# Kernel tuning notes

Hardware: AMD Instinct MI355X
Metric: run time of the kernel (lower is better)

The kernel has to match this reference:

```python
import jax, jax.numpy as jnp
import numpy as np

B, IN_CAPS, IN_DIM = 256, 1152, 8
NUM_CAPS, DIM_VEC = 10, 16
NUM_ROUTING = 3


def squash(v, axis=-1):
    # scale = |v|^2 / (1+|v|^2) / |v|
    s2 = jnp.sum(jnp.square(v), axis=axis, keepdims=True)
    scale = s2 / (1.0 + s2) / jnp.sqrt(s2)
    return scale * v


def setup_inputs() -> dict:
    key = jax.random.key(0)
    k1, k2 = jax.random.split(key)
    inputs = jax.random.normal(k1, (B, IN_CAPS, IN_DIM), dtype=jnp.float32)
    W = jax.random.normal(k2, (IN_CAPS, NUM_CAPS, IN_DIM, DIM_VEC), dtype=jnp.float32) * 0.05
    bias = jnp.zeros((1, IN_CAPS, NUM_CAPS), dtype=jnp.float32)
    return {"inputs": inputs, "W": W, "bias": bias}


def reference(inputs, W, bias):
    # inputs_hat[b,i,j,d] = sum_e inputs[b,i,e] * W[i,j,e,d]
    hat = jnp.einsum('bie,ijed->bijd', inputs, W)  # [B, ic, nc, dv]
    b_logits = bias  # [1, ic, nc], broadcasts to [B, ic, nc] after first update
    outputs = None
    for r in range(NUM_ROUTING):
        c = jax.nn.softmax(b_logits, axis=2)            # coupling over output caps
        s = jnp.sum(c[..., None] * hat, axis=1)         # [B, nc, dv]
        outputs = squash(s)                             # [B, nc, dv]
        if r != NUM_ROUTING - 1:
            # agreement: <hat[b,i,j,:], v[b,j,:]>
            b_logits = b_logits + jnp.einsum('bijd,bjd->bij', hat, outputs)
    return outputs  # [B, num_capsule, dim_vector]
```

## Files before the change

### kernel.cpp

```cpp
#include <hip/hip_runtime.h>
#include <hip/hip_fp16.h>


#define IC 1152
#define IE 8
#define NC 10
#define DV 16
#define NB 256
#define NW (IC * NC * IE * DV)
#define SOUT (NC * DV)
#define GPB (IC / 32)
#define NBB 8
#define TPB (NBB * 64)
#define WSLOT (NC * 8 * 64)

typedef _Float16 h2 __attribute__((ext_vector_type(2)));
union WChunk { int4 v; h2 p[4]; _Float16 h[8]; };
union XFrag { int4 v; h2 p[4]; };

#if defined(__has_builtin) && __has_builtin(__builtin_amdgcn_fdot2)
__device__ inline float fdot2(h2 a, h2 b, float c) {
    return __builtin_amdgcn_fdot2(a, b, c, false);
}
#else
__device__ inline float fdot2(h2 a, h2 b, float c) {
    return fmaf((float)a.x, (float)b.x, fmaf((float)a.y, (float)b.y, c));
}
#endif

__global__ void wprep_kernel(const float* __restrict__ W, int4* __restrict__ Wc) {
    const int t = blockIdx.x * blockDim.x + threadIdx.x;
    if (t >= NW / 8) return;
    const int lane = t & 63;
    const int h = lane >> 5, r = lane & 31;
    const int k = (t >> 6) & 7;
    const int r2 = t >> 9;
    const int j = r2 % NC, Gp = r2 / NC;
    const int i = Gp * 32 + r;
    const int d = h * 8 + k;
    const float* src = W + ((size_t)(i * NC + j) * IE) * DV + d;
    WChunk c;
#pragma unroll
    for (int e = 0; e < IE; ++e) c.h[e] = (_Float16)src[(size_t)e * DV];
    Wc[t] = c.v;
}

__device__ inline void butterfly_store(const float* s8, int r, float* dst8) {
    float t4[4];
#pragma unroll
    for (int d = 0; d < 4; ++d) {
        const bool hi = (r & 16);
        const float mine = hi ? s8[d + 4] : s8[d];
        const float send = hi ? s8[d] : s8[d + 4];
        t4[d] = mine + __shfl_xor(send, 16);
    }
    float t2[2];
#pragma unroll
    for (int d = 0; d < 2; ++d) {
        const bool hi = (r & 8);
        const float mine = hi ? t4[d + 2] : t4[d];
        const float send = hi ? t4[d] : t4[d + 2];
        t2[d] = mine + __shfl_xor(send, 8);
    }
    float t1;
    {
        const bool hi = (r & 4);
        const float mine = hi ? t2[1] : t2[0];
        const float send = hi ? t2[0] : t2[1];
        t1 = mine + __shfl_xor(send, 4);
    }
    t1 += __shfl_xor(t1, 2);
    t1 += __shfl_xor(t1, 1);
    if ((r & 3) == 0) {
        const int dl = (r >> 2) & 7;
        dst8[dl] = t1;
    }
}

template <int RD>
__global__ __launch_bounds__(TPB) void round_caps(
    const float* __restrict__ X,
    const int4* __restrict__ Wc,
    const float* __restrict__ bias,
    const h2* __restrict__ vredH,
    float* __restrict__ sp)
{
    __shared__ __align__(16) int4 Ws[WSLOT];

    const int Gp = blockIdx.x;
    const int bg = blockIdx.y;
    const int tid = threadIdx.x;
    const int w = tid >> 6;
    const int g = tid & 63;
    const int h = g >> 5;
    const int r = g & 31;

    {
        const int4* src = Wc + (size_t)Gp * WSLOT;
#pragma unroll
        for (int k = 0; k < WSLOT / TPB; ++k)
            Ws[tid + k * TPB] = src[tid + k * TPB];
    }

    const int b = bg * NBB + w;
    const int i = Gp * 32 + r;

    XFrag xu;
    {
        const float4* xr = (const float4*)(X + ((size_t)b * IC + i) * IE);
        const float4 x0 = xr[0], x1 = xr[1];
        xu.p[0] = h2{(_Float16)x0.x, (_Float16)x0.y};
        xu.p[1] = h2{(_Float16)x0.z, (_Float16)x0.w};
        xu.p[2] = h2{(_Float16)x1.x, (_Float16)x1.y};
        xu.p[3] = h2{(_Float16)x1.z, (_Float16)x1.w};
    }

    float cj[NC];
    float Z = 0.f;
    if constexpr (RD == 0) {
#pragma unroll
        for (int j = 0; j < NC; ++j) {
            const float e = __expf(bias[i * NC + j]);
            cj[j] = e;
            Z += e;
        }
        const float rz = 1.f / Z;
#pragma unroll
        for (int j = 0; j < NC; ++j) cj[j] *= rz;
    }

    __syncthreads();

    float* spb = sp + ((size_t)Gp * NB + b) * SOUT;

    if constexpr (RD == 0) {
#pragma unroll
        for (int j = 0; j < NC; ++j) {
            const int4* wp = Ws + j * 512 + g;
            float s8[8];
#pragma unroll
            for (int kp = 0; kp < 4; ++kp) {
                WChunk w0, w1;
                w0.v = wp[(2 * kp) * 64];
                w1.v = wp[(2 * kp + 1) * 64];
                float a0 = 0.f, a1 = 0.f;
#pragma unroll
                for (int q = 0; q < 4; ++q) {
                    a0 = fdot2(xu.p[q], w0.p[q], a0);
                    a1 = fdot2(xu.p[q], w1.p[q], a1);
                }
                s8[2 * kp] = cj[j] * a0;
                s8[2 * kp + 1] = cj[j] * a1;
            }
            butterfly_store(s8, r, spb + j * DV + h * 8);
        }
    } else {
        h2 hat2[NC][4];
#pragma unroll
        for (int j = 0; j < NC; ++j) {
            const int4* wp = Ws + j * 512 + g;
#pragma unroll
            for (int kp = 0; kp < 4; ++kp) {
                WChunk w0, w1;
                w0.v = wp[(2 * kp) * 64];
                w1.v = wp[(2 * kp + 1) * 64];
                float a0 = 0.f, a1 = 0.f;
#pragma unroll
                for (int q = 0; q < 4; ++q) {
                    a0 = fdot2(xu.p[q], w0.p[q], a0);
                    a1 = fdot2(xu.p[q], w1.p[q], a1);
                }
                hat2[j][kp] = h2{(_Float16)a0, (_Float16)a1};
            }
            XFrag vv;
            vv.v = *(const int4*)(vredH + (size_t)b * (SOUT / 2) + j * 8 + h * 4);
            float ah = 0.f;
#pragma unroll
            for (int q = 0; q < 4; ++q) ah = fdot2(hat2[j][q], vv.p[q], ah);
            const float lt = bias[i * NC + j] + ah + __shfl_xor(ah, 32);
            const float e = __expf(lt);
            cj[j] = e;
            Z += e;
        }
        const float rz = 1.f / Z;

#pragma unroll
        for (int j = 0; j < NC; ++j) {
            const float cn = cj[j] * rz;
            float s8[8];
#pragma unroll
            for (int q = 0; q < 4; ++q) {
                s8[2 * q]     = cn * (float)hat2[j][q].x;
                s8[2 * q + 1] = cn * (float)hat2[j][q].y;
            }
            butterfly_store(s8, r, spb + j * DV + h * 8);
        }
    }
}

template <int P>
__global__ __launch_bounds__(192) void reduce_caps(
    const float* __restrict__ sp,
    const float* __restrict__ vprevF,
    float* __restrict__ voutF,
    h2* __restrict__ voutH,
    float* __restrict__ out)
{
    const int b = blockIdx.x, t = threadIdx.x;
    if (t >= SOUT) return;
    float sv = 0.f;
#pragma unroll
    for (int gq = 0; gq < GPB; ++gq) sv += sp[((size_t)gq * NB + b) * SOUT + t];
    float s2 = sv * sv;
#pragma unroll
    for (int mk = 8; mk >= 1; mk >>= 1) s2 += __shfl_xor(s2, mk, 16);
    float vv = sqrtf(s2) / (1.f + s2) * sv;
    if constexpr (P == 2) vv += vprevF[(size_t)b * SOUT + t];
    if constexpr (P == 3) {
        out[(size_t)b * SOUT + t] = vv;
        return;
    } else {
        if constexpr (P == 1) voutF[(size_t)b * SOUT + t] = vv;
        const float oth = __shfl_xor(vv, 1);
        if (!(t & 1))
            voutH[(size_t)b * (SOUT / 2) + (t >> 1)] = h2{(_Float16)vv, (_Float16)oth};
    }
}

extern "C" void kernel_launch(void* const* d_in, const int* in_sizes, int n_in,
                              void* d_out, int out_size, void* d_ws, size_t ws_size,
                              hipStream_t stream) {
    const float* X = (const float*)d_in[0];
    const float* W = (const float*)d_in[1];
    const float* bias = (const float*)d_in[2];
    float* out = (float*)d_out;

    int4* Wc = (int4*)d_ws;
    float* spA = (float*)(Wc + NW / 8);
    float* spB = spA + (size_t)GPB * NB * SOUT;
    float* spC = spB + (size_t)GPB * NB * SOUT;
    float* v1F = spC + (size_t)GPB * NB * SOUT;
    h2* vH1 = (h2*)(v1F + (size_t)NB * SOUT);
    h2* vH2 = vH1 + (size_t)NB * (SOUT / 2);

    wprep_kernel<<<dim3(720), dim3(256), 0, stream>>>(W, Wc);

    dim3 rg(GPB, NB / NBB);
    round_caps<0><<<rg, TPB, 0, stream>>>(X, Wc, bias, nullptr, spA);
    reduce_caps<1><<<dim3(NB), dim3(192), 0, stream>>>(spA, nullptr, v1F, vH1, nullptr);
    round_caps<1><<<rg, TPB, 0, stream>>>(X, Wc, bias, vH1, spB);
    reduce_caps<2><<<dim3(NB), dim3(192), 0, stream>>>(spB, v1F, nullptr, vH2, nullptr);
    round_caps<2><<<rg, TPB, 0, stream>>>(X, Wc, bias, vH2, spC);
    reduce_caps<3><<<dim3(NB), dim3(192), 0, stream>>>(spC, nullptr, nullptr, nullptr, out);
}
```

Before: 152.9 us.

## Process two batches per wave in round 0 and use fp32 agreement vectors

Round 0 now has each wave compute two batch rows, so each shared-memory W chunk read is reused twice and the grid is halved. Later rounds read the previous output vector in fp32 with scalar FMAs instead of a packed fp16 copy, so the reduce kernel no longer writes the half-precision vector. A single partial-sum buffer is reused across rounds instead of three. The trade-offs are higher register pressure in round 0 and a little more global traffic for the fp32 vector reads.

```diff
diff --git a/kernel.cpp b/kernel.cpp
--- a/kernel.cpp
+++ b/kernel.cpp
@@ -10,9 +10,11 @@
 #define NW (IC * NC * IE * DV)
 #define SOUT (NC * DV)
 #define GPB (IC / 32)
-#define NBB 8
-#define TPB (NBB * 64)
 #define WSLOT (NC * 8 * 64)
+#define TPB0 512
+#define BPB0 16
+#define TPB1 512
+#define BPB1 8
 
 typedef _Float16 h2 __attribute__((ext_vector_type(2)));
 union WChunk { int4 v; h2 p[4]; _Float16 h[8]; };
@@ -77,47 +79,43 @@
     }
 }
 
-template <int RD>
-__global__ __launch_bounds__(TPB) void round_caps(
-    const float* __restrict__ X,
-    const int4* __restrict__ Wc,
-    const float* __restrict__ bias,
-    const h2* __restrict__ vredH,
-    float* __restrict__ sp)
-{
+__global__ __launch_bounds__(TPB0) void round0_caps(
+    const float* __restrict__ X, const int4* __restrict__ Wc,
+    const float* __restrict__ bias, float* __restrict__ sp) {
     __shared__ __align__(16) int4 Ws[WSLOT];
 
-    const int Gp = blockIdx.x;
-    const int bg = blockIdx.y;
+    const int Gp = blockIdx.x, bg = blockIdx.y;
     const int tid = threadIdx.x;
-    const int w = tid >> 6;
-    const int g = tid & 63;
-    const int h = g >> 5;
-    const int r = g & 31;
+    const int w = tid >> 6, g = tid & 63;
+    const int h = g >> 5, r = g & 31;
 
     {
         const int4* src = Wc + (size_t)Gp * WSLOT;
 #pragma unroll
-        for (int k = 0; k < WSLOT / TPB; ++k)
-            Ws[tid + k * TPB] = src[tid + k * TPB];
-    }
-
-    const int b = bg * NBB + w;
+        for (int k = 0; k < WSLOT / TPB0; ++k)
+            Ws[tid + k * TPB0] = src[tid + k * TPB0];
+    }
+    const int b0 = bg * BPB0 + 2 * w, b1 = b0 + 1;
     const int i = Gp * 32 + r;
 
-    XFrag xu;
-    {
-        const float4* xr = (const float4*)(X + ((size_t)b * IC + i) * IE);
-        const float4 x0 = xr[0], x1 = xr[1];
-        xu.p[0] = h2{(_Float16)x0.x, (_Float16)x0.y};
-        xu.p[1] = h2{(_Float16)x0.z, (_Float16)x0.w};
-        xu.p[2] = h2{(_Float16)x1.x, (_Float16)x1.y};
-        xu.p[3] = h2{(_Float16)x1.z, (_Float16)x1.w};
-    }
-
+    XFrag xu0, xu1;
+    {
+        const float4* xp = (const float4*)(X + ((size_t)b0 * IC + i) * IE);
+        const float4 a0 = xp[0], a1 = xp[1];
+        xu0.p[0] = h2{(_Float16)a0.x, (_Float16)a0.y};
+        xu0.p[1] = h2{(_Float16)a0.z, (_Float16)a0.w};
+        xu0.p[2] = h2{(_Float16)a1.x, (_Float16)a1.y};
+        xu0.p[3] = h2{(_Float16)a1.z, (_Float16)a1.w};
+        const float4* yp = (const float4*)(X + ((size_t)b1 * IC + i) * IE);
+        const float4 c0 = yp[0], c1 = yp[1];
+        xu1.p[0] = h2{(_Float16)c0.x, (_Float16)c0.y};
+        xu1.p[1] = h2{(_Float16)c0.z, (_Float16)c0.w};
+        xu1.p[2] = h2{(_Float16)c1.x, (_Float16)c1.y};
+        xu1.p[3] = h2{(_Float16)c1.z, (_Float16)c1.w};
+    }
     float cj[NC];
-    float Z = 0.f;
-    if constexpr (RD == 0) {
+    {
+        float Z = 0.f;
 #pragma unroll
         for (int j = 0; j < NC; ++j) {
             const float e = __expf(bias[i * NC + j]);
@@ -128,84 +126,116 @@
 #pragma unroll
         for (int j = 0; j < NC; ++j) cj[j] *= rz;
     }
-
     __syncthreads();
 
-    float* spb = sp + ((size_t)Gp * NB + b) * SOUT;
-
-    if constexpr (RD == 0) {
-#pragma unroll
-        for (int j = 0; j < NC; ++j) {
-            const int4* wp = Ws + j * 512 + g;
-            float s8[8];
-#pragma unroll
-            for (int kp = 0; kp < 4; ++kp) {
-                WChunk w0, w1;
-                w0.v = wp[(2 * kp) * 64];
-                w1.v = wp[(2 * kp + 1) * 64];
-                float a0 = 0.f, a1 = 0.f;
-#pragma unroll
-                for (int q = 0; q < 4; ++q) {
-                    a0 = fdot2(xu.p[q], w0.p[q], a0);
-                    a1 = fdot2(xu.p[q], w1.p[q], a1);
-                }
-                s8[2 * kp] = cj[j] * a0;
-                s8[2 * kp + 1] = cj[j] * a1;
+    float* spb0 = sp + ((size_t)Gp * NB + b0) * SOUT + h * 8;
+    float* spb1 = sp + ((size_t)Gp * NB + b1) * SOUT + h * 8;
+#pragma unroll
+    for (int j = 0; j < NC; ++j) {
+        const int4* wp = Ws + j * 512 + g;
+        float s80[8], s81[8];
+#pragma unroll
+        for (int kp = 0; kp < 4; ++kp) {
+            WChunk wa, wb;
+            wa.v = wp[(2 * kp) * 64];
+            wb.v = wp[(2 * kp + 1) * 64];
+            float a00 = 0.f, a01 = 0.f, a10 = 0.f, a11 = 0.f;
+#pragma unroll
+            for (int q = 0; q < 4; ++q) {
+                a00 = fdot2(xu0.p[q], wa.p[q], a00);
+                a01 = fdot2(xu0.p[q], wb.p[q], a01);
+                a10 = fdot2(xu1.p[q], wa.p[q], a10);
+                a11 = fdot2(xu1.p[q], wb.p[q], a11);
             }
-            butterfly_store(s8, r, spb + j * DV + h * 8);
-        }
-    } else {
-        h2 hat2[NC][4];
-#pragma unroll
-        for (int j = 0; j < NC; ++j) {
-            const int4* wp = Ws + j * 512 + g;
-#pragma unroll
-            for (int kp = 0; kp < 4; ++kp) {
-                WChunk w0, w1;
-                w0.v = wp[(2 * kp) * 64];
-                w1.v = wp[(2 * kp + 1) * 64];
-                float a0 = 0.f, a1 = 0.f;
-#pragma unroll
-                for (int q = 0; q < 4; ++q) {
-                    a0 = fdot2(xu.p[q], w0.p[q], a0);
-                    a1 = fdot2(xu.p[q], w1.p[q], a1);
-                }
-                hat2[j][kp] = h2{(_Float16)a0, (_Float16)a1};
+            s80[2 * kp] = cj[j] * a00; s80[2 * kp + 1] = cj[j] * a01;
+            s81[2 * kp] = cj[j] * a10; s81[2 * kp + 1] = cj[j] * a11;
+        }
+        butterfly_store(s80, r, spb0 + j * DV);
+        butterfly_store(s81, r, spb1 + j * DV);
+    }
+}
+
+__global__ __launch_bounds__(TPB1) void roundN_caps(
+    const float* __restrict__ X, const int4* __restrict__ Wc,
+    const float* __restrict__ bias, const float* __restrict__ vF,
+    float* __restrict__ sp) {
+    __shared__ __align__(16) int4 Ws[WSLOT];
+
+    const int Gp = blockIdx.x, bg = blockIdx.y;
+    const int tid = threadIdx.x;
+    const int w = tid >> 6, g = tid & 63;
+    const int h = g >> 5, r = g & 31;
+
+    {
+        const int4* src = Wc + (size_t)Gp * WSLOT;
+#pragma unroll
+        for (int k = 0; k < WSLOT / TPB1; ++k)
+            Ws[tid + k * TPB1] = src[tid + k * TPB1];
+    }
+    const int b = bg * BPB1 + w;
+    const int i = Gp * 32 + r;
+
+    XFrag xu;
+    {
+        const float4* xp = (const float4*)(X + ((size_t)b * IC + i) * IE);
+        const float4 a0 = xp[0], a1 = xp[1];
+        xu.p[0] = h2{(_Float16)a0.x, (_Float16)a0.y};
+        xu.p[1] = h2{(_Float16)a0.z, (_Float16)a0.w};
+        xu.p[2] = h2{(_Float16)a1.x, (_Float16)a1.y};
+        xu.p[3] = h2{(_Float16)a1.z, (_Float16)a1.w};
+    }
+    __syncthreads();
+
+    h2 hat2[NC][4];
+    float cj[NC];
+    float Z = 0.f;
+#pragma unroll
+    for (int j = 0; j < NC; ++j) {
+        const int4* wp = Ws + j * 512 + g;
+#pragma unroll
+        for (int kp = 0; kp < 4; ++kp) {
+            WChunk wa, wb;
+            wa.v = wp[(2 * kp) * 64];
+            wb.v = wp[(2 * kp + 1) * 64];
+            float a0 = 0.f, a1 = 0.f;
+#pragma unroll
+            for (int q = 0; q < 4; ++q) {
+                a0 = fdot2(xu.p[q], wa.p[q], a0);
+                a1 = fdot2(xu.p[q], wb.p[q], a1);
             }
-            XFrag vv;
-            vv.v = *(const int4*)(vredH + (size_t)b * (SOUT / 2) + j * 8 + h * 4);
-            float ah = 0.f;
-#pragma unroll
-            for (int q = 0; q < 4; ++q) ah = fdot2(hat2[j][q], vv.p[q], ah);
-            const float lt = bias[i * NC + j] + ah + __shfl_xor(ah, 32);
-            const float e = __expf(lt);
-            cj[j] = e;
-            Z += e;
-        }
-        const float rz = 1.f / Z;
-
-#pragma unroll
-        for (int j = 0; j < NC; ++j) {
-            const float cn = cj[j] * rz;
-            float s8[8];
-#pragma unroll
-            for (int q = 0; q < 4; ++q) {
-                s8[2 * q]     = cn * (float)hat2[j][q].x;
-                s8[2 * q + 1] = cn * (float)hat2[j][q].y;
-            }
-            butterfly_store(s8, r, spb + j * DV + h * 8);
-        }
+            hat2[j][kp] = h2{(_Float16)a0, (_Float16)a1};
+        }
+        const float4* vp = (const float4*)(vF + (size_t)b * SOUT + j * DV + h * 8);
+        const float4 va = vp[0], vb = vp[1];
+        float ah = (float)hat2[j][0].x * va.x + (float)hat2[j][0].y * va.y +
+                   (float)hat2[j][1].x * va.z + (float)hat2[j][1].y * va.w +
+                   (float)hat2[j][2].x * vb.x + (float)hat2[j][2].y * vb.y +
+                   (float)hat2[j][3].x * vb.z + (float)hat2[j][3].y * vb.w;
+        const float lt = bias[i * NC + j] + ah + __shfl_xor(ah, 32);
+        const float e = __expf(lt);
+        cj[j] = e;
+        Z += e;
+    }
+    const float rz = 1.f / Z;
+
+    float* spb = sp + ((size_t)Gp * NB + b) * SOUT + h * 8;
+#pragma unroll
+    for (int j = 0; j < NC; ++j) {
+        const float cn = cj[j] * rz;
+        float s8[8];
+#pragma unroll
+        for (int q = 0; q < 4; ++q) {
+            s8[2 * q]     = cn * (float)hat2[j][q].x;
+            s8[2 * q + 1] = cn * (float)hat2[j][q].y;
+        }
+        butterfly_store(s8, r, spb + j * DV);
     }
 }
 
 template <int P>
 __global__ __launch_bounds__(192) void reduce_caps(
-    const float* __restrict__ sp,
-    const float* __restrict__ vprevF,
-    float* __restrict__ voutF,
-    h2* __restrict__ voutH,
-    float* __restrict__ out)
-{
+    const float* __restrict__ sp, const float* __restrict__ vprevF,
+    float* __restrict__ voutF, float* __restrict__ out) {
     const int b = blockIdx.x, t = threadIdx.x;
     if (t >= SOUT) return;
     float sv = 0.f;
@@ -216,15 +246,8 @@
     for (int mk = 8; mk >= 1; mk >>= 1) s2 += __shfl_xor(s2, mk, 16);
     float vv = sqrtf(s2) / (1.f + s2) * sv;
     if constexpr (P == 2) vv += vprevF[(size_t)b * SOUT + t];
-    if constexpr (P == 3) {
-        out[(size_t)b * SOUT + t] = vv;
-        return;
-    } else {
-        if constexpr (P == 1) voutF[(size_t)b * SOUT + t] = vv;
-        const float oth = __shfl_xor(vv, 1);
-        if (!(t & 1))
-            voutH[(size_t)b * (SOUT / 2) + (t >> 1)] = h2{(_Float16)vv, (_Float16)oth};
-    }
+    if constexpr (P == 3) out[(size_t)b * SOUT + t] = vv;
+    else voutF[(size_t)b * SOUT + t] = vv;
 }
 
 extern "C" void kernel_launch(void* const* d_in, const int* in_sizes, int n_in,
@@ -236,20 +259,16 @@
     float* out = (float*)d_out;
 
     int4* Wc = (int4*)d_ws;
-    float* spA = (float*)(Wc + NW / 8);
-    float* spB = spA + (size_t)GPB * NB * SOUT;
-    float* spC = spB + (size_t)GPB * NB * SOUT;
-    float* v1F = spC + (size_t)GPB * NB * SOUT;
-    h2* vH1 = (h2*)(v1F + (size_t)NB * SOUT);
-    h2* vH2 = vH1 + (size_t)NB * (SOUT / 2);
+    float* sp = (float*)(Wc + NW / 8);
+    float* v1F = sp + (size_t)GPB * NB * SOUT;
+    float* vsF = v1F + (size_t)NB * SOUT;
 
     wprep_kernel<<<dim3(720), dim3(256), 0, stream>>>(W, Wc);
 
-    dim3 rg(GPB, NB / NBB);
-    round_caps<0><<<rg, TPB, 0, stream>>>(X, Wc, bias, nullptr, spA);
-    reduce_caps<1><<<dim3(NB), dim3(192), 0, stream>>>(spA, nullptr, v1F, vH1, nullptr);
-    round_caps<1><<<rg, TPB, 0, stream>>>(X, Wc, bias, vH1, spB);
-    reduce_caps<2><<<dim3(NB), dim3(192), 0, stream>>>(spB, v1F, nullptr, vH2, nullptr);
-    round_caps<2><<<rg, TPB, 0, stream>>>(X, Wc, bias, vH2, spC);
-    reduce_caps<3><<<dim3(NB), dim3(192), 0, stream>>>(spC, nullptr, nullptr, nullptr, out);
-}
+    round0_caps<<<dim3(GPB, NB / BPB0), TPB0, 0, stream>>>(X, Wc, bias, sp);
+    reduce_caps<1><<<dim3(NB), dim3(192), 0, stream>>>(sp, nullptr, v1F, nullptr);
+    roundN_caps<<<dim3(GPB, NB / BPB1), TPB1, 0, stream>>>(X, Wc, bias, v1F, sp);
+    reduce_caps<2><<<dim3(NB), dim3(192), 0, stream>>>(sp, v1F, vsF, nullptr);
+    roundN_caps<<<dim3(GPB, NB / BPB1), TPB1, 0, stream>>>(X, Wc, bias, vsF, sp);
+    reduce_caps<3><<<dim3(NB), dim3(192), 0, stream>>>(sp, nullptr, nullptr, out);
+}
```

Result: no change. 155.3 us (+1.6%).
